# Performance work log

Hardware: AMD Instinct MI355X
Metric: run time of the kernel (lower is better)

Reference implementation:

```python
import jax, jax.numpy as jnp
import numpy as np

N, E = 50000, 800000
IN_DIM, HID, OUT = 128, 64, 64
NEG_SLOPE = 0.2  # PyG GATConv default leaky_relu slope


def glorot(key, shape):
    fan_in, fan_out = shape[0], shape[-1]
    lim = jnp.sqrt(6.0 / (fan_in + fan_out))
    return jax.random.uniform(key, shape, minval=-lim, maxval=lim, dtype=jnp.float32)


def setup_inputs() -> dict:
    key = jax.random.key(0)
    ks = jax.random.split(key, 10)
    x = jax.random.normal(ks[0], (N, IN_DIM), dtype=jnp.float32)
    edge_index = jax.random.randint(ks[1], (2, E), 0, N, dtype=jnp.int64)
    # GATConv layer 1: heads=2, concat=False
    W1 = glorot(ks[2], (IN_DIM, 2 * HID))
    att_src1 = glorot(ks[3], (1, 2, HID))[0]   # [2, HID]
    att_dst1 = glorot(ks[4], (1, 2, HID))[0]
    b1 = jnp.zeros((HID,), jnp.float32)
    # GATConv layer 2: heads=1, concat=False
    W2 = glorot(ks[5], (HID, OUT))
    att_src2 = glorot(ks[6], (1, 1, OUT))[0]   # [1, OUT]
    att_dst2 = glorot(ks[7], (1, 1, OUT))[0]
    b2 = jnp.zeros((OUT,), jnp.float32)
    return {"x": x, "edge_index": edge_index, "W1": W1, "att_src1": att_src1,
            "att_dst1": att_dst1, "b1": b1, "W2": W2, "att_src2": att_src2,
            "att_dst2": att_dst2, "b2": b2}


def gat_conv(x, src, dst, W, att_src, att_dst, bias, heads, out_ch):
    n = x.shape[0]
    h = (x @ W).reshape(n, heads, out_ch)              # [N,H,C]
    a_src = jnp.einsum('nhc,hc->nh', h, att_src)       # [N,H]
    a_dst = jnp.einsum('nhc,hc->nh', h, att_dst)
    e = jax.nn.leaky_relu(a_src[src] + a_dst[dst], NEG_SLOPE)  # [E,H]
    # softmax over incoming edges per destination node (stable)
    e_max = jax.ops.segment_max(e, dst, num_segments=n)
    ex = jnp.exp(e - e_max[dst])
    denom = jax.ops.segment_sum(ex, dst, num_segments=n)
    alpha = ex / (denom[dst] + 1e-16)                  # [E,H]
    msg = h[src] * alpha[:, :, None]                   # [E,H,C]
    out = jax.ops.segment_sum(msg, dst, num_segments=n)
    return out.mean(axis=1) + bias                     # concat=False -> head mean


def reference(x, edge_index, W1, att_src1, att_dst1, b1, W2, att_src2, att_dst2, b2):
    n = x.shape[0]
    loop = jnp.arange(n, dtype=edge_index.dtype)
    src = jnp.concatenate([edge_index[0], loop])       # PyG add_self_loops
    dst = jnp.concatenate([edge_index[1], loop])
    x1 = gat_conv(x, src, dst, W1, att_src1, att_dst1, b1, 2, HID)
    x1 = jax.nn.elu(x1)
    # eval mode: dropedge and dropout are identity
    out = gat_conv(x1, src, dst, W2, att_src2, att_dst2, b2, 1, OUT)
    return out
```

## Files before the change

kernel.cpp:

```cpp
#include <hip/hip_runtime.h>
#include <math.h>

#define IN_DIM 128
#define HID 64
#define NEG_SLOPE 0.2f
#define CHUNK 4096
#define GCAP 6144
#define SMEM_UNION 53248

typedef __attribute__((ext_vector_type(8))) short bf16x8;
typedef __attribute__((ext_vector_type(4))) float f32x4;
typedef __attribute__((ext_vector_type(2))) float v2f;

__device__ __forceinline__ float wmax(float v){
  #pragma unroll
  for (int o = 32; o > 0; o >>= 1) v = fmaxf(v, __shfl_xor(v, o));
  return v;
}
__device__ __forceinline__ float wsum(float v){
  #pragma unroll
  for (int o = 32; o > 0; o >>= 1) v += __shfl_xor(v, o);
  return v;
}
__device__ __forceinline__ unsigned short f2bf(float f){
  union { float f; unsigned u; } v; v.f = f;
  unsigned r = v.u + 0x7fffu + ((v.u >> 16) & 1u);
  return (unsigned short)(r >> 16);
}
__device__ __forceinline__ float bl(unsigned u){
  union { unsigned u; float f; } v; v.u = u << 16; return v.f;
}
__device__ __forceinline__ float bh(unsigned u){
  union { unsigned u; float f; } v; v.u = u & 0xffff0000u; return v.f;
}
__device__ __forceinline__ v2f up2(unsigned u){
  v2f r; r[0] = bl(u); r[1] = bh(u); return r;
}

__device__ __forceinline__ void incl_scan256(int* sh, int tid){
  #pragma unroll
  for (int off = 1; off < 256; off <<= 1){
    int v = sh[tid];
    if (tid >= off) v += sh[tid - off];
    __syncthreads();
    sh[tid] = v;
    __syncthreads();
  }
}


__device__ void scatter_body(char* smem, const unsigned* __restrict__ packed, int E,
                             const int* __restrict__ binCnt, int* __restrict__ binOff,
                             unsigned* __restrict__ binned, int bx){
  int* ib = (int*)smem;
  int* bc = ib;
  int* lh = ib + 256;
  int* lbase = ib + 512;
  int* gpos = ib + 768;
  int* lcur = ib + 1024;
  unsigned* buf = (unsigned*)(ib + 1280);
  int tid = threadIdx.x;
  int cg = binCnt[tid];
  bc[tid] = cg;
  lh[tid] = 0;
  __syncthreads();
  incl_scan256(bc, tid);
  int binBase_t = bc[tid] - cg;
  int base = bx * CHUNK;
  int rem = E - base;
  unsigned v[CHUNK / 256];
  #pragma unroll
  for (int j = 0; j < CHUNK / 256; j++){
    int i = j * 256 + tid;
    if (i < rem){ v[j] = packed[base + i]; atomicAdd(&lh[v[j] >> 24], 1); }
  }
  __syncthreads();
  lbase[tid] = lh[tid]; __syncthreads();
  incl_scan256(lbase, tid);
  int myExcl = tid ? lbase[tid - 1] : 0;
  __syncthreads();
  lbase[tid] = myExcl;
  lcur[tid] = myExcl;
  if (lh[tid] > 0) gpos[tid] = binBase_t + atomicAdd(&binOff[tid], lh[tid]);
  __syncthreads();
  #pragma unroll
  for (int j = 0; j < CHUNK / 256; j++){
    int i = j * 256 + tid;
    if (i < rem){
      int b = v[j] >> 24;
      int p = atomicAdd(&lcur[b], 1);
      buf[p] = v[j];
    }
  }
  __syncthreads();
  int cn = rem < CHUNK ? rem : CHUNK;
  for (int i = tid; i < cn; i += 256){
    unsigned u = buf[i];
    int b = u >> 24;
    binned[gpos[b] + (i - lbase[b])] = u;
  }
}

__device__ void group_body(char* smem, const unsigned* __restrict__ binned,
                           const int* __restrict__ binCnt, unsigned* __restrict__ sorted,
                           int* __restrict__ row_ptr, int N, int g){
  unsigned* A = (unsigned*)smem;
  unsigned* B = A + GCAP;
  int* ib = (int*)(B + GCAP);
  int* sc = ib;
  int* h2 = ib + 256;
  int* rs = ib + 512;
  int* cur = ib + 768;
  int tid = threadIdx.x;
  int cg = binCnt[tid];
  sc[tid] = cg;
  h2[tid] = 0;
  __syncthreads();
  incl_scan256(sc, tid);
  int base = sc[g] - binCnt[g];
  int cnt = binCnt[g]; if (cnt > GCAP) cnt = GCAP;
  __syncthreads();
  for (int i = tid; i < cnt; i += 256){
    unsigned u = binned[base + i];
    A[i] = u;
    atomicAdd(&h2[(u >> 16) & 255], 1);
  }
  __syncthreads();
  rs[tid] = h2[tid]; __syncthreads();
  incl_scan256(rs, tid);
  int excl = tid ? rs[tid - 1] : 0;
  __syncthreads();
  rs[tid] = excl; cur[tid] = excl;
  int d = g * 256 + tid;
  if (d < N) row_ptr[d] = base + excl;
  __syncthreads();
  for (int i = tid; i < cnt; i += 256){
    unsigned u = A[i];
    int p = atomicAdd(&cur[(u >> 16) & 255], 1);
    B[p] = u;
  }
  __syncthreads();
  for (int i = tid; i < cnt; i += 256)
    sorted[base + i] = B[i];
}

__device__ void gemm1_body(char* smem, const float* __restrict__ X,
                           const unsigned short* __restrict__ Wt,
                           const float* __restrict__ asrc, const float* __restrict__ adst,
                           unsigned short* __restrict__ Hb, float* __restrict__ aa,
                           int n_rows, int n0){
  const int KP = 136, CP = 132;
  unsigned short* xa = (unsigned short*)smem;
  unsigned short* wl = xa + 64 * KP;
  int tid = threadIdx.x;
  for (int idx = tid; idx < 64 * 32; idx += 256){
    int n = idx >> 5, k4 = idx & 31;
    float4 v = make_float4(0.f, 0.f, 0.f, 0.f);
    if (n0 + n < n_rows) v = *(const float4*)&X[(size_t)(n0 + n) * 128 + k4 * 4];
    ushort4 pk; pk.x = f2bf(v.x); pk.y = f2bf(v.y); pk.z = f2bf(v.z); pk.w = f2bf(v.w);
    *(ushort4*)&xa[n * KP + k4 * 4] = pk;
  }
  for (int idx = tid; idx < 128 * 16; idx += 256){
    int n = idx >> 4, k8 = idx & 15;
    uint4 v = *(const uint4*)&Wt[(size_t)n * 128 + k8 * 8];
    *(uint4*)&wl[n * KP + k8 * 8] = v;
  }
  __syncthreads();

  int lane = tid & 63, w = tid >> 6;
  int m = lane & 15, q = lane >> 4;
  f32x4 acc[4][2];
  #pragma unroll
  for (int i = 0; i < 4; i++)
    #pragma unroll
    for (int j = 0; j < 2; j++)
      #pragma unroll
      for (int r = 0; r < 4; r++) acc[i][j][r] = 0.f;
  #pragma unroll
  for (int ks = 0; ks < 4; ks++){
    bf16x8 bg[2];
    #pragma unroll
    for (int j = 0; j < 2; j++)
      bg[j] = *(const bf16x8*)&wl[((2 * w + j) * 16 + m) * KP + ks * 32 + q * 8];
    #pragma unroll
    for (int i = 0; i < 4; i++){
      bf16x8 af = *(const bf16x8*)&xa[(i * 16 + m) * KP + ks * 32 + q * 8];
      #pragma unroll
      for (int j = 0; j < 2; j++)
        acc[i][j] = __builtin_amdgcn_mfma_f32_16x16x32_bf16(af, bg[j], acc[i][j], 0, 0, 0);
    }
  }
  __syncthreads();
  float* C = (float*)smem;
  #pragma unroll
  for (int i = 0; i < 4; i++)
    #pragma unroll
    for (int j = 0; j < 2; j++)
      #pragma unroll
      for (int r = 0; r < 4; r++)
        C[(i * 16 + q * 4 + r) * CP + (2 * w + j) * 16 + m] = acc[i][j][r];
  __syncthreads();

  int row = tid >> 2;
  int c0 = (tid & 3) * 32;
  int n = n0 + row;
  int head = (tid & 3) >> 1;
  float s_p = 0.f, d_p = 0.f;
  unsigned short hb[32];
  #pragma unroll
  for (int c = 0; c < 32; c += 4){
    f32x4 v = *(const f32x4*)&C[row * CP + c0 + c];
    #pragma unroll
    for (int u = 0; u < 4; u++){
      int ch = (c0 + c + u) & 63;
      s_p += v[u] * asrc[head * 64 + ch];
      d_p += v[u] * adst[head * 64 + ch];
      hb[c + u] = f2bf(v[u]);
    }
  }
  if (n < n_rows){
    #pragma unroll
    for (int c = 0; c < 32; c += 8){
      uint4 pk;
      pk.x = (unsigned)hb[c]     | ((unsigned)hb[c + 1] << 16);
      pk.y = (unsigned)hb[c + 2] | ((unsigned)hb[c + 3] << 16);
      pk.z = (unsigned)hb[c + 4] | ((unsigned)hb[c + 5] << 16);
      pk.w = (unsigned)hb[c + 6] | ((unsigned)hb[c + 7] << 16);
      *(uint4*)&Hb[(size_t)n * 128 + c0 + c] = pk;
    }
  }
  s_p += __shfl_xor(s_p, 1);
  d_p += __shfl_xor(d_p, 1);
  if ((tid & 1) == 0 && n < n_rows){
    aa[(size_t)n * 4 + head]     = s_p;
    aa[(size_t)n * 4 + 2 + head] = d_p;
  }
}


__global__ __launch_bounds__(256) void sort_gemm_a(const unsigned* __restrict__ packed, int E,
    const int* __restrict__ binCnt, int* __restrict__ binOff, unsigned* __restrict__ binned,
    int NS, const float* __restrict__ X, const unsigned short* __restrict__ W1t,
    const float* __restrict__ asrc1, const float* __restrict__ adst1,
    unsigned short* __restrict__ h1b, float* __restrict__ aa1, int n_rows){
  __shared__ char smem[SMEM_UNION];
  int bx = blockIdx.x;
  if (bx < NS){
    scatter_body(smem, packed, E, binCnt, binOff, binned, bx);
  } else {
    gemm1_body(smem, X, W1t, asrc1, adst1, h1b, aa1, n_rows, (bx - NS) * 64);
  }
}

__global__ __launch_bounds__(256) void sort_gemm_b(const unsigned* __restrict__ binned,
    const int* __restrict__ binCnt, unsigned* __restrict__ sorted, int* __restrict__ row_ptr,
    int N, int NS, int gofs, const float* __restrict__ X, const unsigned short* __restrict__ W1t,
    const float* __restrict__ asrc1, const float* __restrict__ adst1,
    unsigned short* __restrict__ h1b, float* __restrict__ aa1, int n_rows){
  __shared__ char smem[SMEM_UNION];
  int bx = blockIdx.x;
  if (bx < NS){
    group_body(smem, binned, binCnt, sorted, row_ptr, N, bx);
  } else {
    gemm1_body(smem, X, W1t, asrc1, adst1, h1b, aa1, n_rows, (gofs + bx - NS) * 64);
  }
}


__global__ __launch_bounds__(256) void prep(const int* __restrict__ ei, int E, int NBLK,
                                            unsigned* __restrict__ packed,
                                            int* __restrict__ binCnt,
                                            const float* __restrict__ W1,
                                            const float* __restrict__ W2,
                                            unsigned short* __restrict__ W1t,
                                            unsigned short* __restrict__ W2t,
                                            int* __restrict__ row_ptr, int N){
  int tid = threadIdx.x;
  if ((int)blockIdx.x < NBLK){
    __shared__ int lh[256];
    lh[tid] = 0; __syncthreads();
    int base = blockIdx.x * CHUNK;
    #pragma unroll
    for (int j = 0; j < CHUNK / 256; j++){
      int e = base + j * 256 + tid;
      if (e < E){
        unsigned s = (unsigned)ei[e];
        unsigned d = (unsigned)ei[E + e];
        packed[e] = (d << 16) | s;
        atomicAdd(&lh[d >> 8], 1);
      }
    }
    __syncthreads();
    if (lh[tid] > 0) atomicAdd(&binCnt[tid], lh[tid]);
  } else {
    int t = (blockIdx.x - NBLK) * 256 + tid;
    if (t < 128 * 128){
      int n = t >> 7, k = t & 127;
      W1t[n * 128 + k] = f2bf(W1[k * 128 + n]);
    }
    int t2 = t - 128 * 128;
    if (t2 >= 0 && t2 < 64 * 64){
      int n = t2 >> 6, k = t2 & 63;
      W2t[n * 64 + k] = f2bf(W2[k * 64 + n]);
    }
    if (t == 0) row_ptr[N] = E;
  }
}


template<int K, int NC, int HEADS>
__global__ __launch_bounds__(512) void gemm_mfma(const float* __restrict__ X,
    const unsigned short* __restrict__ Wt, const float* __restrict__ asrc,
    const float* __restrict__ adst, unsigned short* __restrict__ Hb,
    float* __restrict__ aa, int n_rows)
{
  constexpr int MT = 128;
  constexpr int KP = K + 8;
  constexpr int CP = NC + 4;
  constexpr int MF = MT / 16;
  constexpr int NFt = NC / 16;
  constexpr int WPN = 8 / NFt;
  constexpr int MFW = MF / WPN;
  constexpr unsigned SM1 = (unsigned)(MT + NC) * KP * 2;
  constexpr unsigned SM2 = (unsigned)MT * CP * 4;
  __shared__ char smem[SM1 > SM2 ? SM1 : SM2];
  unsigned short* xa = (unsigned short*)smem;
  unsigned short* wl = xa + MT * KP;
  int tid = threadIdx.x;
  int n0 = blockIdx.x * MT;

  for (int idx = tid; idx < MT * (K / 4); idx += 512){
    int n = idx / (K / 4), k4 = idx % (K / 4);
    float4 v = make_float4(0.f, 0.f, 0.f, 0.f);
    if (n0 + n < n_rows) v = *(const float4*)&X[(size_t)(n0 + n) * K + k4 * 4];
    ushort4 pk; pk.x = f2bf(v.x); pk.y = f2bf(v.y); pk.z = f2bf(v.z); pk.w = f2bf(v.w);
    *(ushort4*)&xa[n * KP + k4 * 4] = pk;
  }
  for (int idx = tid; idx < NC * (K / 8); idx += 512){
    int n = idx / (K / 8), k8 = idx % (K / 8);
    uint4 v = *(const uint4*)&Wt[(size_t)n * K + k8 * 8];
    *(uint4*)&wl[n * KP + k8 * 8] = v;
  }
  __syncthreads();

  int lane = tid & 63, w = tid >> 6;
  int m = lane & 15, q = lane >> 4;
  int nf = w % NFt;
  int mseg = w / NFt;
  f32x4 acc[MFW];
  #pragma unroll
  for (int i = 0; i < MFW; i++)
    #pragma unroll
    for (int r = 0; r < 4; r++) acc[i][r] = 0.f;

  #pragma unroll
  for (int ks = 0; ks < K / 32; ks++){
    bf16x8 bg = *(const bf16x8*)&wl[(nf * 16 + m) * KP + ks * 32 + q * 8];
    #pragma unroll
    for (int i = 0; i < MFW; i++){
      bf16x8 af = *(const bf16x8*)&xa[((mseg * MFW + i) * 16 + m) * KP + ks * 32 + q * 8];
      acc[i] = __builtin_amdgcn_mfma_f32_16x16x32_bf16(af, bg, acc[i], 0, 0, 0);
    }
  }
  __syncthreads();
  float* C = (float*)smem;
  #pragma unroll
  for (int i = 0; i < MFW; i++)
    #pragma unroll
    for (int r = 0; r < 4; r++)
      C[((mseg * MFW + i) * 16 + q * 4 + r) * CP + nf * 16 + m] = acc[i][r];
  __syncthreads();

  constexpr int CH = NC / 4;
  int row = tid >> 2;
  int c0 = (tid & 3) * CH;
  int n = n0 + row;
  int head = (HEADS == 2) ? (c0 >> 6) : 0;
  float s_p = 0.f, d_p = 0.f;
  unsigned short hb[CH];
  #pragma unroll
  for (int c = 0; c < CH; c += 4){
    f32x4 v = *(const f32x4*)&C[row * CP + c0 + c];
    #pragma unroll
    for (int u = 0; u < 4; u++){
      int ch = (c0 + c + u) & 63;
      s_p += v[u] * asrc[head * 64 + ch];
      d_p += v[u] * adst[head * 64 + ch];
      hb[c + u] = f2bf(v[u]);
    }
  }
  if (n < n_rows){
    #pragma unroll
    for (int c = 0; c < CH; c += 8){
      uint4 pk;
      pk.x = (unsigned)hb[c]     | ((unsigned)hb[c + 1] << 16);
      pk.y = (unsigned)hb[c + 2] | ((unsigned)hb[c + 3] << 16);
      pk.z = (unsigned)hb[c + 4] | ((unsigned)hb[c + 5] << 16);
      pk.w = (unsigned)hb[c + 6] | ((unsigned)hb[c + 7] << 16);
      *(uint4*)&Hb[(size_t)n * NC + c0 + c] = pk;
    }
  }
  s_p += __shfl_xor(s_p, 1);
  d_p += __shfl_xor(d_p, 1);
  if (HEADS == 2){
    if ((tid & 1) == 0 && n < n_rows){
      aa[(size_t)n * 4 + head]     = s_p;
      aa[(size_t)n * 4 + 2 + head] = d_p;
    }
  } else {
    s_p += __shfl_xor(s_p, 2);
    d_p += __shfl_xor(d_p, 2);
    if ((tid & 3) == 0 && n < n_rows){
      aa[(size_t)n * 2]     = s_p;
      aa[(size_t)n * 2 + 1] = d_p;
    }
  }
}


__global__ void agg_layer1(const int* __restrict__ row_ptr, const unsigned* __restrict__ sorted,
                           const float* __restrict__ aa, const unsigned short* __restrict__ h1b,
                           const float* __restrict__ b1, float* __restrict__ x1, int n_nodes){
  int d = (blockIdx.x * blockDim.x + threadIdx.x) >> 6;
  int lane = threadIdx.x & 63;
  if (d >= n_nodes) return;
  int rp0 = row_ptr[d];
  int deg = row_ptr[d + 1] - rp0;
  float2 adv = *(const float2*)&aa[d * 4 + 2];
  int s = -1;
  if (lane < deg) s = (int)(sorted[rp0 + lane] & 0xffffu);
  else if (lane == deg) s = d;
  float e0 = -INFINITY, e1 = -INFINITY;
  if (s >= 0){
    float2 asv = *(const float2*)&aa[s * 4];
    float t0 = asv.x + adv.x;
    float t1 = asv.y + adv.y;
    e0 = t0 >= 0.f ? t0 : NEG_SLOPE * t0;
    e1 = t1 >= 0.f ? t1 : NEG_SLOPE * t1;
  }
  float m0 = wmax(e0), m1 = wmax(e1);
  float p0 = (s >= 0) ? __expf(e0 - m0) : 0.f;
  float p1 = (s >= 0) ? __expf(e1 - m1) : 0.f;
  float al0 = p0 / (wsum(p0) + 1e-16f);
  float al1 = p1 / (wsum(p1) + 1e-16f);
  int ne = deg + 1;
  int g = lane >> 4, c = lane & 15;
  v2f acc[4] = {{0.f,0.f},{0.f,0.f},{0.f,0.f},{0.f,0.f}};
  #pragma unroll 2
  for (int j0 = 0; j0 < ne; j0 += 4){
    int j = j0 + g;
    int sj = __shfl(s, j);
    float a0 = __shfl(al0, j);
    float a1 = __shfl(al1, j);
    if (j < ne){
      uint4 v = ((const uint4*)(h1b + (size_t)sj * 128))[c];
      float a = (c < 8) ? a0 : a1;
      v2f av = {a, a};
      acc[0] = av * up2(v.x) + acc[0];
      acc[1] = av * up2(v.y) + acc[1];
      acc[2] = av * up2(v.z) + acc[2];
      acc[3] = av * up2(v.w) + acc[3];
    }
  }
  float accf[8] = {acc[0][0], acc[0][1], acc[1][0], acc[1][1],
                   acc[2][0], acc[2][1], acc[3][0], acc[3][1]};
  #pragma unroll
  for (int i = 0; i < 8; i++){
    accf[i] += __shfl_xor(accf[i], 16);
    accf[i] += __shfl_xor(accf[i], 32);
  }
  float outv[8];
  #pragma unroll
  for (int i = 0; i < 8; i++){
    float o = __shfl_xor(accf[i], 8);
    outv[i] = 0.5f * (accf[i] + o);
  }
  if (g == 0 && c < 8){
    float r[8];
    #pragma unroll
    for (int i = 0; i < 8; i++){
      float v = outv[i] + b1[c * 8 + i];
      r[i] = v > 0.f ? v : expm1f(v);
    }
    float* p = &x1[(size_t)d * 64 + c * 8];
    *(float4*)p       = make_float4(r[0], r[1], r[2], r[3]);
    *(float4*)(p + 4) = make_float4(r[4], r[5], r[6], r[7]);
  }
}

__global__ void agg_layer2(const int* __restrict__ row_ptr, const unsigned* __restrict__ sorted,
                           const float* __restrict__ aa, const unsigned short* __restrict__ h2b,
                           const float* __restrict__ b2, float* __restrict__ out, int n_nodes){
  int d = (blockIdx.x * blockDim.x + threadIdx.x) >> 6;
  int lane = threadIdx.x & 63;
  if (d >= n_nodes) return;
  int rp0 = row_ptr[d];
  int deg = row_ptr[d + 1] - rp0;
  float ad = aa[d * 2 + 1];
  int s = -1;
  if (lane < deg) s = (int)(sorted[rp0 + lane] & 0xffffu);
  else if (lane == deg) s = d;
  float e = -INFINITY;
  if (s >= 0){
    float t = aa[s * 2 + 0] + ad;
    e = t >= 0.f ? t : NEG_SLOPE * t;
  }
  float m = wmax(e);
  float p = (s >= 0) ? __expf(e - m) : 0.f;
  float al = p / (wsum(p) + 1e-16f);
  int ne = deg + 1;
  int g = lane >> 3, c = lane & 7;
  v2f acc[4] = {{0.f,0.f},{0.f,0.f},{0.f,0.f},{0.f,0.f}};
  #pragma unroll 2
  for (int j0 = 0; j0 < ne; j0 += 8){
    int j = j0 + g;
    int sj = __shfl(s, j);
    float a = __shfl(al, j);
    if (j < ne){
      uint4 v = ((const uint4*)(h2b + (size_t)sj * 64))[c];
      v2f av = {a, a};
      acc[0] = av * up2(v.x) + acc[0];
      acc[1] = av * up2(v.y) + acc[1];
      acc[2] = av * up2(v.z) + acc[2];
      acc[3] = av * up2(v.w) + acc[3];
    }
  }
  float accf[8] = {acc[0][0], acc[0][1], acc[1][0], acc[1][1],
                   acc[2][0], acc[2][1], acc[3][0], acc[3][1]};
  #pragma unroll
  for (int i = 0; i < 8; i++){
    accf[i] += __shfl_xor(accf[i], 8);
    accf[i] += __shfl_xor(accf[i], 16);
    accf[i] += __shfl_xor(accf[i], 32);
  }
  if (lane < 8){
    float r[8];
    #pragma unroll
    for (int i = 0; i < 8; i++) r[i] = accf[i] + b2[lane * 8 + i];
    float* q = &out[(size_t)d * 64 + lane * 8];
    *(float4*)q       = make_float4(r[0], r[1], r[2], r[3]);
    *(float4*)(q + 4) = make_float4(r[4], r[5], r[6], r[7]);
  }
}

extern "C" void kernel_launch(void* const* d_in, const int* in_sizes, int n_in,
                              void* d_out, int out_size, void* d_ws, size_t ws_size,
                              hipStream_t stream){
  const float* x     = (const float*)d_in[0];
  const int*   ei    = (const int*)d_in[1];
  const float* W1    = (const float*)d_in[2];
  const float* asrc1 = (const float*)d_in[3];
  const float* adst1 = (const float*)d_in[4];
  const float* b1    = (const float*)d_in[5];
  const float* W2    = (const float*)d_in[6];
  const float* asrc2 = (const float*)d_in[7];
  const float* adst2 = (const float*)d_in[8];
  const float* b2    = (const float*)d_in[9];
  float* out = (float*)d_out;
  int N = in_sizes[0] / IN_DIM;
  int E = in_sizes[1] / 2;
  int NG = (N + 255) >> 8;
  int NBLK = (E + CHUNK - 1) / CHUNK;
  int ngrp = (N + 3) / 4;
  int GT = (N + 63) / 64;
  int GA = GT / 2;
  int GB = GT - GA;

  char* p = (char*)d_ws;
  unsigned short* h1b = (unsigned short*)p;  p += (size_t)N * 128 * 2;
  unsigned short* h2b = (unsigned short*)p;  p += (size_t)N * 64 * 2;
  float* x1  = (float*)p;                    p += (size_t)N * 64 * 4;
  float* aa1 = (float*)p;                    p += (size_t)N * 4 * 4;
  float* aa2 = (float*)p;                    p += (size_t)N * 2 * 4;
  unsigned* packed = (unsigned*)p;           p += (size_t)E * 4;
  unsigned* binned = (unsigned*)p;           p += (size_t)E * 4;
  unsigned* sorted = (unsigned*)p;           p += (size_t)E * 4;
  int* row_ptr   = (int*)p;                  p += (size_t)(N + 1) * 4;
  int* binCnt    = (int*)p;                  p += 256 * 4;
  int* binOff    = (int*)p;                  p += 256 * 4;
  unsigned short* W1t = (unsigned short*)p;  p += 128 * 128 * 2;
  unsigned short* W2t = (unsigned short*)p;

  hipMemsetAsync(binCnt, 0, 512 * sizeof(int), stream);
  prep<<<NBLK + 80, 256, 0, stream>>>(ei, E, NBLK, packed, binCnt,
                                      W1, W2, W1t, W2t, row_ptr, N);
  sort_gemm_a<<<NBLK + GA, 256, 0, stream>>>(packed, E, binCnt, binOff, binned,
                                             NBLK, x, W1t, asrc1, adst1, h1b, aa1, N);
  sort_gemm_b<<<NG + GB, 256, 0, stream>>>(binned, binCnt, sorted, row_ptr, N,
                                           NG, GA, x, W1t, asrc1, adst1, h1b, aa1, N);
  agg_layer1<<<ngrp, 256, 0, stream>>>(row_ptr, sorted, aa1, h1b, b1, x1, N);
  gemm_mfma<64, 64, 1><<<(N + 127) / 128, 512, 0, stream>>>(
      x1, W2t, asrc2, adst2, h2b, aa2, N);
  agg_layer2<<<ngrp, 256, 0, stream>>>(row_ptr, sorted, aa2, h2b, b2, out, N);
}
```

Measured before the change: 238.1 us.

## Store layer-1 output as bf16 and batch gather loads in aggregation kernels

Layer-1 aggregation now writes its ELU output as bf16 instead of fp32, and the second GEMM reads that bf16 directly. This halves the intermediate write and read traffic and drops the float-to-bf16 conversion in the GEMM load. Both aggregation loops now issue four independent neighbor-row loads before doing the FMAs, so more memory requests are in flight. Block size goes from 256 to 512 threads. The precision of x1 is unchanged in effect, because the GEMM already rounded it to bf16 before.

```diff
diff --git a/kernel.cpp b/kernel.cpp
--- a/kernel.cpp
+++ b/kernel.cpp
@@ -143,6 +143,7 @@
   for (int i = tid; i < cnt; i += 256)
     sorted[base + i] = B[i];
 }
+
 
 __device__ void gemm1_body(char* smem, const float* __restrict__ X,
                            const unsigned short* __restrict__ Wt,
@@ -308,19 +309,17 @@
 }
 
 
-template<int K, int NC, int HEADS>
-__global__ __launch_bounds__(512) void gemm_mfma(const float* __restrict__ X,
+__global__ __launch_bounds__(512) void gemm2_mfma(const unsigned short* __restrict__ Xb,
     const unsigned short* __restrict__ Wt, const float* __restrict__ asrc,
     const float* __restrict__ adst, unsigned short* __restrict__ Hb,
     float* __restrict__ aa, int n_rows)
 {
+  constexpr int K = 64, NC = 64;
   constexpr int MT = 128;
   constexpr int KP = K + 8;
   constexpr int CP = NC + 4;
-  constexpr int MF = MT / 16;
   constexpr int NFt = NC / 16;
-  constexpr int WPN = 8 / NFt;
-  constexpr int MFW = MF / WPN;
+  constexpr int MFW = (MT / 16) / (8 / NFt);
   constexpr unsigned SM1 = (unsigned)(MT + NC) * KP * 2;
   constexpr unsigned SM2 = (unsigned)MT * CP * 4;
   __shared__ char smem[SM1 > SM2 ? SM1 : SM2];
@@ -329,15 +328,14 @@
   int tid = threadIdx.x;
   int n0 = blockIdx.x * MT;
 
-  for (int idx = tid; idx < MT * (K / 4); idx += 512){
-    int n = idx / (K / 4), k4 = idx % (K / 4);
-    float4 v = make_float4(0.f, 0.f, 0.f, 0.f);
-    if (n0 + n < n_rows) v = *(const float4*)&X[(size_t)(n0 + n) * K + k4 * 4];
-    ushort4 pk; pk.x = f2bf(v.x); pk.y = f2bf(v.y); pk.z = f2bf(v.z); pk.w = f2bf(v.w);
-    *(ushort4*)&xa[n * KP + k4 * 4] = pk;
+  for (int idx = tid; idx < MT * (K / 8); idx += 512){
+    int n = idx >> 3, k8 = idx & 7;
+    uint4 v = make_uint4(0u, 0u, 0u, 0u);
+    if (n0 + n < n_rows) v = *(const uint4*)&Xb[(size_t)(n0 + n) * K + k8 * 8];
+    *(uint4*)&xa[n * KP + k8 * 8] = v;
   }
   for (int idx = tid; idx < NC * (K / 8); idx += 512){
-    int n = idx / (K / 8), k8 = idx % (K / 8);
+    int n = idx >> 3, k8 = idx & 7;
     uint4 v = *(const uint4*)&Wt[(size_t)n * K + k8 * 8];
     *(uint4*)&wl[n * KP + k8 * 8] = v;
   }
@@ -345,8 +343,8 @@
 
   int lane = tid & 63, w = tid >> 6;
   int m = lane & 15, q = lane >> 4;
-  int nf = w % NFt;
-  int mseg = w / NFt;
+  int nf = w & 3;
+  int mseg = w >> 2;
   f32x4 acc[MFW];
   #pragma unroll
   for (int i = 0; i < MFW; i++)
@@ -375,7 +373,6 @@
   int row = tid >> 2;
   int c0 = (tid & 3) * CH;
   int n = n0 + row;
-  int head = (HEADS == 2) ? (c0 >> 6) : 0;
   float s_p = 0.f, d_p = 0.f;
   unsigned short hb[CH];
   #pragma unroll
@@ -384,8 +381,8 @@
     #pragma unroll
     for (int u = 0; u < 4; u++){
       int ch = (c0 + c + u) & 63;
-      s_p += v[u] * asrc[head * 64 + ch];
-      d_p += v[u] * adst[head * 64 + ch];
+      s_p += v[u] * asrc[ch];
+      d_p += v[u] * adst[ch];
       hb[c + u] = f2bf(v[u]);
     }
   }
@@ -402,25 +399,20 @@
   }
   s_p += __shfl_xor(s_p, 1);
   d_p += __shfl_xor(d_p, 1);
-  if (HEADS == 2){
-    if ((tid & 1) == 0 && n < n_rows){
-      aa[(size_t)n * 4 + head]     = s_p;
-      aa[(size_t)n * 4 + 2 + head] = d_p;
-    }
-  } else {
-    s_p += __shfl_xor(s_p, 2);
-    d_p += __shfl_xor(d_p, 2);
-    if ((tid & 3) == 0 && n < n_rows){
-      aa[(size_t)n * 2]     = s_p;
-      aa[(size_t)n * 2 + 1] = d_p;
-    }
-  }
-}
-
-
-__global__ void agg_layer1(const int* __restrict__ row_ptr, const unsigned* __restrict__ sorted,
+  s_p += __shfl_xor(s_p, 2);
+  d_p += __shfl_xor(d_p, 2);
+  if ((tid & 3) == 0 && n < n_rows){
+    aa[(size_t)n * 2]     = s_p;
+    aa[(size_t)n * 2 + 1] = d_p;
+  }
+}
+
+
+__global__ __launch_bounds__(512) void agg_layer1(const int* __restrict__ row_ptr,
+                           const unsigned* __restrict__ sorted,
                            const float* __restrict__ aa, const unsigned short* __restrict__ h1b,
-                           const float* __restrict__ b1, float* __restrict__ x1, int n_nodes){
+                           const float* __restrict__ b1, unsigned short* __restrict__ x1b,
+                           int n_nodes){
   int d = (blockIdx.x * blockDim.x + threadIdx.x) >> 6;
   int lane = threadIdx.x & 63;
   if (d >= n_nodes) return;
@@ -445,21 +437,29 @@
   float al1 = p1 / (wsum(p1) + 1e-16f);
   int ne = deg + 1;
   int g = lane >> 4, c = lane & 15;
+  bool hsel = (c < 8);
+  const uint4* hp = (const uint4*)h1b;
   v2f acc[4] = {{0.f,0.f},{0.f,0.f},{0.f,0.f},{0.f,0.f}};
-  #pragma unroll 2
-  for (int j0 = 0; j0 < ne; j0 += 4){
-    int j = j0 + g;
-    int sj = __shfl(s, j);
-    float a0 = __shfl(al0, j);
-    float a1 = __shfl(al1, j);
-    if (j < ne){
-      uint4 v = ((const uint4*)(h1b + (size_t)sj * 128))[c];
-      float a = (c < 8) ? a0 : a1;
-      v2f av = {a, a};
-      acc[0] = av * up2(v.x) + acc[0];
-      acc[1] = av * up2(v.y) + acc[1];
-      acc[2] = av * up2(v.z) + acc[2];
-      acc[3] = av * up2(v.w) + acc[3];
+  for (int j0 = 0; j0 < ne; j0 += 16){
+    uint4 v[4]; float av[4];
+    #pragma unroll
+    for (int b = 0; b < 4; b++){
+      int j = j0 + b * 4 + g;
+      int sj = __shfl(s, j);
+      float a0 = __shfl(al0, j);
+      float a1 = __shfl(al1, j);
+      av[b] = hsel ? a0 : a1;
+      if (j < ne) v[b] = hp[sj * 16 + c];
+    }
+    #pragma unroll
+    for (int b = 0; b < 4; b++){
+      if (j0 + b * 4 + g < ne){
+        v2f aw = {av[b], av[b]};
+        acc[0] = aw * up2(v[b].x) + acc[0];
+        acc[1] = aw * up2(v[b].y) + acc[1];
+        acc[2] = aw * up2(v[b].z) + acc[2];
+        acc[3] = aw * up2(v[b].w) + acc[3];
+      }
     }
   }
   float accf[8] = {acc[0][0], acc[0][1], acc[1][0], acc[1][1],
@@ -476,19 +476,24 @@
     outv[i] = 0.5f * (accf[i] + o);
   }
   if (g == 0 && c < 8){
-    float r[8];
+    unsigned short hb[8];
     #pragma unroll
     for (int i = 0; i < 8; i++){
       float v = outv[i] + b1[c * 8 + i];
-      r[i] = v > 0.f ? v : expm1f(v);
-    }
-    float* p = &x1[(size_t)d * 64 + c * 8];
-    *(float4*)p       = make_float4(r[0], r[1], r[2], r[3]);
-    *(float4*)(p + 4) = make_float4(r[4], r[5], r[6], r[7]);
-  }
-}
-
-__global__ void agg_layer2(const int* __restrict__ row_ptr, const unsigned* __restrict__ sorted,
+      float r = v > 0.f ? v : expm1f(v);
+      hb[i] = f2bf(r);
+    }
+    uint4 pk;
+    pk.x = (unsigned)hb[0] | ((unsigned)hb[1] << 16);
+    pk.y = (unsigned)hb[2] | ((unsigned)hb[3] << 16);
+    pk.z = (unsigned)hb[4] | ((unsigned)hb[5] << 16);
+    pk.w = (unsigned)hb[6] | ((unsigned)hb[7] << 16);
+    *(uint4*)&x1b[(size_t)d * 64 + c * 8] = pk;
+  }
+}
+
+__global__ __launch_bounds__(512) void agg_layer2(const int* __restrict__ row_ptr,
+                           const unsigned* __restrict__ sorted,
                            const float* __restrict__ aa, const unsigned short* __restrict__ h2b,
                            const float* __restrict__ b2, float* __restrict__ out, int n_nodes){
   int d = (blockIdx.x * blockDim.x + threadIdx.x) >> 6;
@@ -510,19 +515,26 @@
   float al = p / (wsum(p) + 1e-16f);
   int ne = deg + 1;
   int g = lane >> 3, c = lane & 7;
+  const uint4* hp = (const uint4*)h2b;
   v2f acc[4] = {{0.f,0.f},{0.f,0.f},{0.f,0.f},{0.f,0.f}};
-  #pragma unroll 2
-  for (int j0 = 0; j0 < ne; j0 += 8){
-    int j = j0 + g;
-    int sj = __shfl(s, j);
-    float a = __shfl(al, j);
-    if (j < ne){
-      uint4 v = ((const uint4*)(h2b + (size_t)sj * 64))[c];
-      v2f av = {a, a};
-      acc[0] = av * up2(v.x) + acc[0];
-      acc[1] = av * up2(v.y) + acc[1];
-      acc[2] = av * up2(v.z) + acc[2];
-      acc[3] = av * up2(v.w) + acc[3];
+  for (int j0 = 0; j0 < ne; j0 += 32){
+    uint4 v[4]; float av[4];
+    #pragma unroll
+    for (int b = 0; b < 4; b++){
+      int j = j0 + b * 8 + g;
+      int sj = __shfl(s, j);
+      av[b] = __shfl(al, j);
+      if (j < ne) v[b] = hp[sj * 8 + c];
+    }
+    #pragma unroll
+    for (int b = 0; b < 4; b++){
+      if (j0 + b * 8 + g < ne){
+        v2f aw = {av[b], av[b]};
+        acc[0] = aw * up2(v[b].x) + acc[0];
+        acc[1] = aw * up2(v[b].y) + acc[1];
+        acc[2] = aw * up2(v[b].z) + acc[2];
+        acc[3] = aw * up2(v[b].w) + acc[3];
+      }
     }
   }
   float accf[8] = {acc[0][0], acc[0][1], acc[1][0], acc[1][1],
@@ -561,7 +573,7 @@
   int E = in_sizes[1] / 2;
   int NG = (N + 255) >> 8;
   int NBLK = (E + CHUNK - 1) / CHUNK;
-  int ngrp = (N + 3) / 4;
+  int nagg = (N + 7) / 8;
   int GT = (N + 63) / 64;
   int GA = GT / 2;
   int GB = GT - GA;
@@ -569,7 +581,7 @@
   char* p = (char*)d_ws;
   unsigned short* h1b = (unsigned short*)p;  p += (size_t)N * 128 * 2;
   unsigned short* h2b = (unsigned short*)p;  p += (size_t)N * 64 * 2;
-  float* x1  = (float*)p;                    p += (size_t)N * 64 * 4;
+  unsigned short* x1b = (unsigned short*)p;  p += (size_t)N * 64 * 2;
   float* aa1 = (float*)p;                    p += (size_t)N * 4 * 4;
   float* aa2 = (float*)p;                    p += (size_t)N * 2 * 4;
   unsigned* packed = (unsigned*)p;           p += (size_t)E * 4;
@@ -588,8 +600,7 @@
                                              NBLK, x, W1t, asrc1, adst1, h1b, aa1, N);
   sort_gemm_b<<<NG + GB, 256, 0, stream>>>(binned, binCnt, sorted, row_ptr, N,
                                            NG, GA, x, W1t, asrc1, adst1, h1b, aa1, N);
-  agg_layer1<<<ngrp, 256, 0, stream>>>(row_ptr, sorted, aa1, h1b, b1, x1, N);
-  gemm_mfma<64, 64, 1><<<(N + 127) / 128, 512, 0, stream>>>(
-      x1, W2t, asrc2, adst2, h2b, aa2, N);
-  agg_layer2<<<ngrp, 256, 0, stream>>>(row_ptr, sorted, aa2, h2b, b2, out, N);
-}
+  agg_layer1<<<nagg, 512, 0, stream>>>(row_ptr, sorted, aa1, h1b, b1, x1b, N);
+  gemm2_mfma<<<(N + 127) / 128, 512, 0, stream>>>(x1b, W2t, asrc2, adst2, h2b, aa2, N);
+  agg_layer2<<<nagg, 512, 0, stream>>>(row_ptr, sorted, aa2, h2b, b2, out, N);
+}
```

After: 237.4 us. Within noise of the previous version (-0.3%).
